# Performance work log

Measured on AMD Instinct MI355X. Metric: run time of the kernel, lower is better.

The kernel has to match this reference:

```python
import jax, jax.numpy as jnp
import numpy as np

N = 262144      # number of tokens/nodes
E = 262144      # number of dependency edges (~1 per token)
D_IN = 128
D_OUT = 128
L = 32          # number of dependency labels
R = 2 + 2 * L   # 'self', 'root', L forward labels, L reversed labels
SELF = 0        # index of 'self' weight


def setup_inputs() -> dict:
    key = jax.random.key(0)
    k1, k2, k3, k4, k5 = jax.random.split(key, 5)
    x = jax.random.normal(k1, (N, D_IN), dtype=jnp.float32)
    dep_idx = jax.random.randint(k2, (E,), 0, N)
    gov_idx = jax.random.randint(k3, (E,), 0, N)
    # edges grouped by relation label: labels occupy weight slots [2, 2+L)
    rel_idx = 2 + jnp.repeat(jnp.arange(L), E // L)
    # stacked Linear params: W[r] is [in, out] (== torch weight.T), b[r] is [out]
    W = jax.random.normal(k4, (R, D_IN, D_OUT), dtype=jnp.float32) / np.sqrt(D_IN)
    b = jax.random.normal(k5, (R, D_OUT), dtype=jnp.float32) * 0.01
    return {"x": x, "W": W, "b": b, "dep_idx": dep_idx,
            "gov_idx": gov_idx, "rel_idx": rel_idx}


def reference(x, W, b, dep_idx, gov_idx, rel_idx):
    n = x.shape[0]
    e = dep_idx.shape[0]
    eg = e // L  # edges per relation group (rel_idx is grouped/sorted)

    Wf, bf = W[2:2 + L], b[2:2 + L]           # forward-relation weights
    Wr, br = W[2 + L:2 + 2 * L], b[2 + L:]    # reversed-relation weights

    # forward messages: governor -> dependent, per-relation grouped GEMM
    xg = x[gov_idx].reshape(L, eg, D_IN)                      # [L, eg, in]
    msg_f = jnp.einsum('rei,rio->reo', xg, Wf) + bf[:, None]  # [L, eg, out]
    agg_f = jax.ops.segment_sum(msg_f.reshape(e, D_OUT), dep_idx,
                                num_segments=n)

    # reversed messages: dependent -> governor
    xd = x[dep_idx].reshape(L, eg, D_IN)
    msg_r = jnp.einsum('rei,rio->reo', xd, Wr) + br[:, None]
    agg_r = jax.ops.segment_sum(msg_r.reshape(e, D_OUT), gov_idx,
                                num_segments=n)

    # self transform for every token
    self_t = x @ W[SELF] + b[SELF]

    return jax.nn.relu(self_t + agg_f + agg_r)
```

## Files before the change

kernel.cpp:

```cpp
#include <hip/hip_runtime.h>
#include <hip/hip_bf16.h>
#include <stdint.h>

#define D_DIM 128
#define L_REL 32
#define MSG_LDW 132
#define CPB 4

typedef __attribute__((ext_vector_type(8))) short short8;
typedef __attribute__((ext_vector_type(4))) float f32x4;

__device__ __forceinline__ unsigned short f2bf(float f) {
    union { float f; unsigned u; } v; v.f = f;
    unsigned r = v.u + 0x7FFFu + ((v.u >> 16) & 1u);
    return (unsigned short)(r >> 16);
}
__device__ __forceinline__ float bf_lo(unsigned m) { return __uint_as_float(m << 16); }
__device__ __forceinline__ float bf_hi(unsigned m) { return __uint_as_float(m & 0xffff0000u); }

__device__ __forceinline__ void load_wfrag(const float* __restrict__ Wr,
                                           int w, int l15, int lq,
                                           short8 wf[2][4]) {
#pragma unroll
    for (int n = 0; n < 2; ++n) {
        int c = (w * 2 + n) * 16 + l15;
#pragma unroll
        for (int kk = 0; kk < 4; ++kk) {
            int kb = kk * 32 + lq * 8;
            short8 f;
#pragma unroll
            for (int j = 0; j < 8; ++j)
                f[j] = (short)f2bf(Wr[(size_t)(kb + j) * D_DIM + c]);
            wf[n][kk] = f;
        }
    }
}

__device__ __forceinline__ void mfma_tile(const unsigned short* xs,
                                          const short8 wf[2][4],
                                          int l15, int lq, f32x4 acc[4][2]) {
#pragma unroll
    for (int kk = 0; kk < 4; ++kk) {
        short8 a[4];
#pragma unroll
        for (int m = 0; m < 4; ++m) {
            int row = m * 16 + l15;
            unsigned byte = ((unsigned)(row * 256 + (kk * 32 + lq * 8) * 2))
                          ^ (((unsigned)(row & 7)) << 4);
            a[m] = *reinterpret_cast<const short8*>(
                       reinterpret_cast<const char*>(xs) + byte);
        }
#pragma unroll
        for (int m = 0; m < 4; ++m)
#pragma unroll
            for (int n = 0; n < 2; ++n)
                acc[m][n] = __builtin_amdgcn_mfma_f32_16x16x32_bf16(
                                a[m], wf[n][kk], acc[m][n], 0, 0, 0);
    }
}

__global__ void hist_kernel(const int* __restrict__ dep, const int* __restrict__ gov,
                            int* __restrict__ deg, int E) {
    int i = blockIdx.x * blockDim.x + threadIdx.x;
    int stride = gridDim.x * blockDim.x;
    for (; i < E; i += stride) {
        atomicAdd(&deg[dep[i]], 1);
        atomicAdd(&deg[gov[i]], 1);
    }
}

__global__ __launch_bounds__(256) void scanA_kernel(const int* __restrict__ deg,
                                                    int* __restrict__ off,
                                                    int* __restrict__ partials) {
    __shared__ int ls[256];
    const int tid = threadIdx.x;
    const int gi = blockIdx.x * 256 + tid;
    int4 v = ((const int4*)deg)[gi];
    int s = v.x + v.y + v.z + v.w;
    ls[tid] = s;
    __syncthreads();
    for (int o = 1; o < 256; o <<= 1) {
        int t = (tid >= o) ? ls[tid - o] : 0;
        __syncthreads();
        ls[tid] += t;
        __syncthreads();
    }
    int e0 = ls[tid] - s;
    int4 e; e.x = e0; e.y = e0 + v.x; e.z = e.y + v.y; e.w = e.z + v.z;
    ((int4*)off)[gi] = e;
    if (tid == 255) partials[blockIdx.x] = ls[255];
}

__global__ __launch_bounds__(256) void scanB_kernel(int* __restrict__ partials) {
    __shared__ int ls[256];
    const int tid = threadIdx.x;
    int v = partials[tid];
    ls[tid] = v;
    __syncthreads();
    for (int o = 1; o < 256; o <<= 1) {
        int t = (tid >= o) ? ls[tid - o] : 0;
        __syncthreads();
        ls[tid] += t;
        __syncthreads();
    }
    partials[tid] = ls[tid] - v;
}

__global__ __launch_bounds__(256) void scanC_kernel(int* __restrict__ off,
                                                    int* __restrict__ cur,
                                                    const int* __restrict__ partials) {
    const int p = partials[blockIdx.x];
    const int gi = blockIdx.x * 256 + threadIdx.x;
    int4 v = ((int4*)off)[gi];
    v.x += p; v.y += p; v.z += p; v.w += p;
    ((int4*)off)[gi] = v;
    ((int4*)cur)[gi] = v;
}

__global__ __launch_bounds__(256) void msg_kernel(const float* __restrict__ x,
                                                  const float* __restrict__ W,
                                                  const float* __restrict__ b,
                                                  const int* __restrict__ dep,
                                                  const int* __restrict__ gov,
                                                  int* __restrict__ cur,
                                                  unsigned* __restrict__ msg,
                                                  int eg, int blocksPerRel) {
    __shared__ __align__(16) unsigned short xs[64 * 128];
    __shared__ __align__(16) unsigned short tr[64 * MSG_LDW];
    __shared__ int sidx[CPB][64];
    __shared__ int didx[CPB][64];
    __shared__ int pos[64];

    const int tid = threadIdx.x;
    const int lane = tid & 63, w = tid >> 6;
    const int l15 = lane & 15, lq = lane >> 4;

    const int bid = blockIdx.x;
    const int vr = bid / blocksPerRel;
    const int blk = bid % blocksPerRel;
    const int r = vr & 31;
    const bool fwd = (vr < 32);
    const int* __restrict__ srcI = fwd ? gov : dep;
    const int* __restrict__ dstI = fwd ? dep : gov;

    const int ebase0 = r * eg + blk * CPB * 64;
    {
        int c = tid >> 6, t = tid & 63;
        sidx[c][t] = srcI[ebase0 + c * 64 + t];
        didx[c][t] = dstI[ebase0 + c * 64 + t];
    }

    short8 wf[2][4];
    load_wfrag(W + (size_t)(2 + vr) * D_DIM * D_DIM, w, l15, lq, wf);
    float bias[2];
#pragma unroll
    for (int n = 0; n < 2; ++n)
        bias[n] = b[(size_t)(2 + vr) * D_DIM + (w * 2 + n) * 16 + l15];

    const int srow = tid >> 5;
    const int sf4  = tid & 31;
    __syncthreads();

    float4 st[8];
#pragma unroll
    for (int it = 0; it < 8; ++it) {
        int row = it * 8 + srow;
        st[it] = *reinterpret_cast<const float4*>(
                     x + (size_t)sidx[0][row] * D_DIM + sf4 * 4);
    }
#pragma unroll
    for (int it = 0; it < 8; ++it) {
        int row = it * 8 + srow;
        unsigned lo = (unsigned)f2bf(st[it].x) | ((unsigned)f2bf(st[it].y) << 16);
        unsigned hi = (unsigned)f2bf(st[it].z) | ((unsigned)f2bf(st[it].w) << 16);
        unsigned byte = ((unsigned)(row * 256 + sf4 * 8))
                      ^ (((unsigned)(row & 7)) << 4);
        *reinterpret_cast<uint2*>(reinterpret_cast<char*>(xs) + byte) =
            make_uint2(lo, hi);
    }
    __syncthreads();

    for (int ch = 0; ch < CPB; ++ch) {
        float4 nx[8];
        if (ch + 1 < CPB) {
#pragma unroll
            for (int it = 0; it < 8; ++it) {
                int row = it * 8 + srow;
                nx[it] = *reinterpret_cast<const float4*>(
                             x + (size_t)sidx[ch + 1][row] * D_DIM + sf4 * 4);
            }
        }

        f32x4 acc[4][2];
#pragma unroll
        for (int m = 0; m < 4; ++m)
#pragma unroll
            for (int n = 0; n < 2; ++n) acc[m][n] = (f32x4){0.f, 0.f, 0.f, 0.f};
        mfma_tile(xs, wf, l15, lq, acc);

        if (tid < 64) pos[tid] = atomicAdd(&cur[didx[ch][tid]], 1);

#pragma unroll
        for (int m = 0; m < 4; ++m)
#pragma unroll
            for (int reg = 0; reg < 4; ++reg) {
                int row = m * 16 + lq * 4 + reg;
#pragma unroll
                for (int n = 0; n < 2; ++n)
                    tr[row * MSG_LDW + w * 32 + n * 16 + l15] =
                        f2bf(acc[m][n][reg] + bias[n]);
            }
        __syncthreads();

#pragma unroll
        for (int i = 0; i < 16; ++i) {
            int r0 = w * 16 + i;
            unsigned dw = *reinterpret_cast<const unsigned*>(
                              reinterpret_cast<const char*>(tr)
                              + r0 * MSG_LDW * 2 + lane * 4);
            msg[(size_t)pos[r0] * 64 + lane] = dw;
        }
        if (ch + 1 < CPB) {
#pragma unroll
            for (int it = 0; it < 8; ++it) {
                int row = it * 8 + srow;
                unsigned lo = (unsigned)f2bf(nx[it].x) | ((unsigned)f2bf(nx[it].y) << 16);
                unsigned hi = (unsigned)f2bf(nx[it].z) | ((unsigned)f2bf(nx[it].w) << 16);
                unsigned byte = ((unsigned)(row * 256 + sf4 * 8))
                              ^ (((unsigned)(row & 7)) << 4);
                *reinterpret_cast<uint2*>(reinterpret_cast<char*>(xs) + byte) =
                    make_uint2(lo, hi);
            }
            __syncthreads();
        }
    }
}

__global__ __launch_bounds__(256) void agg_kernel(const float* __restrict__ x,
                                                  const float* __restrict__ W,
                                                  const float* __restrict__ b,
                                                  const int* __restrict__ off,
                                                  const int* __restrict__ deg,
                                                  const unsigned* __restrict__ msg,
                                                  float* __restrict__ out) {
    __shared__ __align__(16) char smem[64 * MSG_LDW * 2];
    unsigned short* xs = (unsigned short*)smem;
    unsigned short* st = (unsigned short*)smem;
    __shared__ int offs[64 + 1];

    const int tid = threadIdx.x;
    const int lane = tid & 63, w = tid >> 6;
    const int l15 = lane & 15, lq = lane >> 4;
    const int base = blockIdx.x * 64;

    if (tid < 64) offs[tid] = off[base + tid];
    if (tid == 64) offs[64] = off[base + 63] + deg[base + 63];

    short8 wf[2][4];
    load_wfrag(W, w, l15, lq, wf);
    float bias[2];
#pragma unroll
    for (int n = 0; n < 2; ++n) bias[n] = b[(w * 2 + n) * 16 + l15];

#pragma unroll
    for (int it = 0; it < 8; ++it) {
        int flat = it * 256 + tid;
        int row = flat >> 5, f4 = flat & 31;
        float4 v = *reinterpret_cast<const float4*>(
                       x + (size_t)(base + row) * D_DIM + f4 * 4);
        unsigned lo = (unsigned)f2bf(v.x) | ((unsigned)f2bf(v.y) << 16);
        unsigned hi = (unsigned)f2bf(v.z) | ((unsigned)f2bf(v.w) << 16);
        unsigned byte = ((unsigned)(row * 256 + f4 * 8))
                      ^ (((unsigned)(row & 7)) << 4);
        *reinterpret_cast<uint2*>(reinterpret_cast<char*>(xs) + byte) =
            make_uint2(lo, hi);
    }
    __syncthreads();

    f32x4 acc[4][2];
#pragma unroll
    for (int m = 0; m < 4; ++m)
#pragma unroll
        for (int n = 0; n < 2; ++n) acc[m][n] = (f32x4){0.f, 0.f, 0.f, 0.f};
    mfma_tile(xs, wf, l15, lq, acc);
    __syncthreads();

#pragma unroll
    for (int m = 0; m < 4; ++m)
#pragma unroll
        for (int reg = 0; reg < 4; ++reg) {
            int row = m * 16 + lq * 4 + reg;
#pragma unroll
            for (int n = 0; n < 2; ++n)
                st[row * MSG_LDW + w * 32 + n * 16 + l15] =
                    f2bf(acc[m][n][reg] + bias[n]);
        }
    __syncthreads();

    const int nfirst = w * 16;
    int ci = 0;
    float2 accm = make_float2(0.f, 0.f);

#define FLUSH_NODE()                                                          \
    do {                                                                      \
        const unsigned sv = *reinterpret_cast<const unsigned*>(               \
            reinterpret_cast<const char*>(st)                                 \
            + (nfirst + ci) * MSG_LDW * 2 + lane * 4);                        \
        float2 so;                                                            \
        so.x = fmaxf(bf_lo(sv) + accm.x, 0.f);                                \
        so.y = fmaxf(bf_hi(sv) + accm.y, 0.f);                                \
        *reinterpret_cast<float2*>(                                           \
            out + (size_t)(base + nfirst + ci) * D_DIM + lane * 2) = so;      \
        accm.x = 0.f; accm.y = 0.f;                                           \
        ++ci;                                                                 \
    } while (0)

    const int s0 = offs[nfirst];
    const int s1 = offs[nfirst + 16];
    int nb = offs[nfirst + 1];
    int j = s0;
    const unsigned* mp = msg + (size_t)j * 64 + lane;

    for (; j + 16 <= s1; j += 16, mp += 1024) {
        unsigned v[16];
#pragma unroll
        for (int k = 0; k < 16; ++k) v[k] = mp[k * 64];
#pragma unroll
        for (int k = 0; k < 16; ++k) {
            int jj = j + k;
            while (jj >= nb) { FLUSH_NODE(); nb = offs[nfirst + ci + 1]; }
            accm.x += bf_lo(v[k]); accm.y += bf_hi(v[k]);
        }
    }
    for (; j < s1; ++j, mp += 64) {
        unsigned v = mp[0];
        while (j >= nb) { FLUSH_NODE(); nb = offs[nfirst + ci + 1]; }
        accm.x += bf_lo(v); accm.y += bf_hi(v);
    }
    while (ci < 16) FLUSH_NODE();
#undef FLUSH_NODE
}

__global__ __launch_bounds__(256) void self_kernel(const float* __restrict__ x,
                                                   const float* __restrict__ W,
                                                   const float* __restrict__ b,
                                                   float* __restrict__ out) {
    __shared__ unsigned short xs[64 * D_DIM];
    const int tid = threadIdx.x;
    const int lane = tid & 63, w = tid >> 6;
    const int l15 = lane & 15, lq = lane >> 4;
    short8 wf[2][4];
    load_wfrag(W, w, l15, lq, wf);
    float bias[2];
#pragma unroll
    for (int n = 0; n < 2; ++n) bias[n] = b[(w * 2 + n) * 16 + l15];
    const int rbase = blockIdx.x * 64;
#pragma unroll
    for (int it = 0; it < 8; ++it) {
        int flat = it * 256 + tid;
        int row = flat >> 5, f4 = flat & 31;
        float4 v = *reinterpret_cast<const float4*>(
                       x + (size_t)(rbase + row) * D_DIM + f4 * 4);
        unsigned lo = (unsigned)f2bf(v.x) | ((unsigned)f2bf(v.y) << 16);
        unsigned hi = (unsigned)f2bf(v.z) | ((unsigned)f2bf(v.w) << 16);
        unsigned byte = ((unsigned)(row * 256 + f4 * 8))
                      ^ (((unsigned)(row & 7)) << 4);
        *reinterpret_cast<uint2*>(reinterpret_cast<char*>(xs) + byte) =
            make_uint2(lo, hi);
    }
    __syncthreads();
    f32x4 acc[4][2];
#pragma unroll
    for (int m = 0; m < 4; ++m)
#pragma unroll
        for (int n = 0; n < 2; ++n) acc[m][n] = (f32x4){0.f, 0.f, 0.f, 0.f};
    mfma_tile(xs, wf, l15, lq, acc);
#pragma unroll
    for (int m = 0; m < 4; ++m)
#pragma unroll
        for (int reg = 0; reg < 4; ++reg) {
            int row = rbase + m * 16 + lq * 4 + reg;
#pragma unroll
            for (int n = 0; n < 2; ++n) {
                int c = (w * 2 + n) * 16 + l15;
                out[(size_t)row * D_DIM + c] = acc[m][n][reg] + bias[n];
            }
        }
}

__global__ __launch_bounds__(256) void edge_kernel(const float* __restrict__ x,
                                                   const float* __restrict__ W,
                                                   const float* __restrict__ b,
                                                   const int* __restrict__ dep,
                                                   const int* __restrict__ gov,
                                                   float* __restrict__ out,
                                                   int eg, int blocksPerRel) {
    __shared__ unsigned short xs[64 * D_DIM];
    __shared__ int sidx[CPB][64];
    __shared__ int didx[CPB][64];
    const int tid = threadIdx.x;
    const int lane = tid & 63, w = tid >> 6;
    const int l15 = lane & 15, lq = lane >> 4;
    const int bid = blockIdx.x;
    const int vr = bid / blocksPerRel;
    const int blk = bid % blocksPerRel;
    const int r = vr & 31;
    const bool fwd = (vr < 32);
    const int* __restrict__ srcI = fwd ? gov : dep;
    const int* __restrict__ dstI = fwd ? dep : gov;
    const int ebase0 = r * eg + blk * CPB * 64;
    {
        int c = tid >> 6, t = tid & 63;
        sidx[c][t] = srcI[ebase0 + c * 64 + t];
        didx[c][t] = dstI[ebase0 + c * 64 + t];
    }
    short8 wf[2][4];
    load_wfrag(W + (size_t)(2 + vr) * D_DIM * D_DIM, w, l15, lq, wf);
    float bias[2];
#pragma unroll
    for (int n = 0; n < 2; ++n)
        bias[n] = b[(size_t)(2 + vr) * D_DIM + (w * 2 + n) * 16 + l15];
    __syncthreads();
#pragma unroll
    for (int ch = 0; ch < CPB; ++ch) {
#pragma unroll
        for (int it = 0; it < 8; ++it) {
            int flat = it * 256 + tid;
            int row = flat >> 5, f4 = flat & 31;
            float4 v = *reinterpret_cast<const float4*>(
                           x + (size_t)sidx[ch][row] * D_DIM + f4 * 4);
            unsigned lo = (unsigned)f2bf(v.x) | ((unsigned)f2bf(v.y) << 16);
            unsigned hi = (unsigned)f2bf(v.z) | ((unsigned)f2bf(v.w) << 16);
            unsigned byte = ((unsigned)(row * 256 + f4 * 8))
                          ^ (((unsigned)(row & 7)) << 4);
            *reinterpret_cast<uint2*>(reinterpret_cast<char*>(xs) + byte) =
                make_uint2(lo, hi);
        }
        __syncthreads();
        f32x4 acc[4][2];
#pragma unroll
        for (int m = 0; m < 4; ++m)
#pragma unroll
            for (int n = 0; n < 2; ++n) acc[m][n] = (f32x4){0.f, 0.f, 0.f, 0.f};
        mfma_tile(xs, wf, l15, lq, acc);
#pragma unroll
        for (int m = 0; m < 4; ++m)
#pragma unroll
            for (int reg = 0; reg < 4; ++reg) {
                int erow = m * 16 + lq * 4 + reg;
                int dst = didx[ch][erow];
#pragma unroll
                for (int n = 0; n < 2; ++n) {
                    int c = (w * 2 + n) * 16 + l15;
                    unsafeAtomicAdd(&out[(size_t)dst * D_DIM + c],
                                    acc[m][n][reg] + bias[n]);
                }
            }
        __syncthreads();
    }
}

__global__ void relu_kernel(float* __restrict__ o, int n4) {
    int i = blockIdx.x * blockDim.x + threadIdx.x;
    int stride = gridDim.x * blockDim.x;
    float4* p = reinterpret_cast<float4*>(o);
    for (; i < n4; i += stride) {
        float4 v = p[i];
        v.x = fmaxf(v.x, 0.f); v.y = fmaxf(v.y, 0.f);
        v.z = fmaxf(v.z, 0.f); v.w = fmaxf(v.w, 0.f);
        p[i] = v;
    }
}

extern "C" void kernel_launch(void* const* d_in, const int* in_sizes, int n_in,
                              void* d_out, int out_size, void* d_ws, size_t ws_size,
                              hipStream_t stream) {
    const float* x   = (const float*)d_in[0];
    const float* W   = (const float*)d_in[1];
    const float* b   = (const float*)d_in[2];
    const int*   dep = (const int*)d_in[3];
    const int*   gov = (const int*)d_in[4];
    float* out = (float*)d_out;

    const int N  = in_sizes[0] / D_DIM;
    const int E  = in_sizes[3];
    const int eg = E / L_REL;

    const size_t msgBytes = (size_t)2 * E * 64 * sizeof(unsigned);
    const size_t need = msgBytes + (size_t)(3 * N + 256) * 4 + 4096;

    const int blocksPerRel = eg / 64 / CPB;

    if (ws_size >= need) {
        char* basep = (char*)d_ws;
        unsigned* msg = (unsigned*)basep;
        int* deg = (int*)(basep + msgBytes);
        int* off = deg + (size_t)N;
        int* cur = off + (size_t)N;
        int* partials = cur + (size_t)N;

        hipMemsetAsync(deg, 0, (size_t)N * sizeof(int), stream);
        hist_kernel<<<512, 256, 0, stream>>>(dep, gov, deg, E);
        scanA_kernel<<<N / 1024, 256, 0, stream>>>(deg, off, partials);
        scanB_kernel<<<1, 256, 0, stream>>>(partials);
        scanC_kernel<<<N / 1024, 256, 0, stream>>>(off, cur, partials);

        msg_kernel<<<64 * blocksPerRel, 256, 0, stream>>>(x, W, b, dep, gov,
                                                          cur, msg, eg,
                                                          blocksPerRel);
        agg_kernel<<<N / 64, 256, 0, stream>>>(x, W, b, off, deg, msg, out);
    } else {
        self_kernel<<<N / 64, 256, 0, stream>>>(x, W, b, out);
        edge_kernel<<<64 * blocksPerRel, 256, 0, stream>>>(x, W, b, dep, gov, out,
                                                           eg, blocksPerRel);
        relu_kernel<<<2048, 256, 0, stream>>>(out, out_size / 4);
    }
}
```

Measured before the change: 213.7 us.

## Write messages straight from MFMA registers and double-buffer staging in msg kernel

The message kernel drops the LDS transpose buffer and writes packed bf16 pairs directly from MFMA accumulators to the global message array, using a permuted column order. The x staging tile is double-buffered and the slot atomics for the next chunk are issued early, which removes one barrier per chunk. The aggregation kernel reads the same permuted layout, with its self-transform tile packed the same way and outputs written as scalar floats at permuted columns. The aim is fewer LDS round trips and syncs, at the cost of less coalesced 4-byte global stores and double the LDS for x.

```diff
diff --git a/kernel.cpp b/kernel.cpp
--- a/kernel.cpp
+++ b/kernel.cpp
@@ -4,7 +4,7 @@
 
 #define D_DIM 128
 #define L_REL 32
-#define MSG_LDW 132
+#define ST_LDW 66
 #define CPB 4
 
 typedef __attribute__((ext_vector_type(8))) short short8;
@@ -125,11 +125,10 @@
                                                   int* __restrict__ cur,
                                                   unsigned* __restrict__ msg,
                                                   int eg, int blocksPerRel) {
-    __shared__ __align__(16) unsigned short xs[64 * 128];
-    __shared__ __align__(16) unsigned short tr[64 * MSG_LDW];
+    __shared__ __align__(16) unsigned short xs[2][64 * 128];
     __shared__ int sidx[CPB][64];
     __shared__ int didx[CPB][64];
-    __shared__ int pos[64];
+    __shared__ int pos[2][64];
 
     const int tid = threadIdx.x;
     const int lane = tid & 63, w = tid >> 6;
@@ -161,26 +160,31 @@
     const int sf4  = tid & 31;
     __syncthreads();
 
-    float4 st[8];
-#pragma unroll
-    for (int it = 0; it < 8; ++it) {
-        int row = it * 8 + srow;
-        st[it] = *reinterpret_cast<const float4*>(
-                     x + (size_t)sidx[0][row] * D_DIM + sf4 * 4);
-    }
-#pragma unroll
-    for (int it = 0; it < 8; ++it) {
-        int row = it * 8 + srow;
-        unsigned lo = (unsigned)f2bf(st[it].x) | ((unsigned)f2bf(st[it].y) << 16);
-        unsigned hi = (unsigned)f2bf(st[it].z) | ((unsigned)f2bf(st[it].w) << 16);
-        unsigned byte = ((unsigned)(row * 256 + sf4 * 8))
-                      ^ (((unsigned)(row & 7)) << 4);
-        *reinterpret_cast<uint2*>(reinterpret_cast<char*>(xs) + byte) =
-            make_uint2(lo, hi);
+    {
+        float4 st0[8];
+#pragma unroll
+        for (int it = 0; it < 8; ++it) {
+            int row = it * 8 + srow;
+            st0[it] = *reinterpret_cast<const float4*>(
+                          x + (size_t)sidx[0][row] * D_DIM + sf4 * 4);
+        }
+#pragma unroll
+        for (int it = 0; it < 8; ++it) {
+            int row = it * 8 + srow;
+            unsigned lo = (unsigned)f2bf(st0[it].x) | ((unsigned)f2bf(st0[it].y) << 16);
+            unsigned hi = (unsigned)f2bf(st0[it].z) | ((unsigned)f2bf(st0[it].w) << 16);
+            unsigned byte = ((unsigned)(row * 256 + sf4 * 8))
+                          ^ (((unsigned)(row & 7)) << 4);
+            *reinterpret_cast<uint2*>(reinterpret_cast<char*>(xs[0]) + byte) =
+                make_uint2(lo, hi);
+        }
+        if (tid < 64) pos[0][tid] = atomicAdd(&cur[didx[0][tid]], 1);
     }
     __syncthreads();
 
     for (int ch = 0; ch < CPB; ++ch) {
+        const int cb = ch & 1;
+
         float4 nx[8];
         if (ch + 1 < CPB) {
 #pragma unroll
@@ -196,30 +200,18 @@
         for (int m = 0; m < 4; ++m)
 #pragma unroll
             for (int n = 0; n < 2; ++n) acc[m][n] = (f32x4){0.f, 0.f, 0.f, 0.f};
-        mfma_tile(xs, wf, l15, lq, acc);
-
-        if (tid < 64) pos[tid] = atomicAdd(&cur[didx[ch][tid]], 1);
+        mfma_tile(xs[cb], wf, l15, lq, acc);
 
 #pragma unroll
         for (int m = 0; m < 4; ++m)
 #pragma unroll
             for (int reg = 0; reg < 4; ++reg) {
                 int row = m * 16 + lq * 4 + reg;
-#pragma unroll
-                for (int n = 0; n < 2; ++n)
-                    tr[row * MSG_LDW + w * 32 + n * 16 + l15] =
-                        f2bf(acc[m][n][reg] + bias[n]);
+                unsigned dw = (unsigned)f2bf(acc[m][0][reg] + bias[0])
+                            | ((unsigned)f2bf(acc[m][1][reg] + bias[1]) << 16);
+                msg[(size_t)pos[cb][row] * 64 + w * 16 + l15] = dw;
             }
-        __syncthreads();
-
-#pragma unroll
-        for (int i = 0; i < 16; ++i) {
-            int r0 = w * 16 + i;
-            unsigned dw = *reinterpret_cast<const unsigned*>(
-                              reinterpret_cast<const char*>(tr)
-                              + r0 * MSG_LDW * 2 + lane * 4);
-            msg[(size_t)pos[r0] * 64 + lane] = dw;
-        }
+
         if (ch + 1 < CPB) {
 #pragma unroll
             for (int it = 0; it < 8; ++it) {
@@ -228,9 +220,10 @@
                 unsigned hi = (unsigned)f2bf(nx[it].z) | ((unsigned)f2bf(nx[it].w) << 16);
                 unsigned byte = ((unsigned)(row * 256 + sf4 * 8))
                               ^ (((unsigned)(row & 7)) << 4);
-                *reinterpret_cast<uint2*>(reinterpret_cast<char*>(xs) + byte) =
+                *reinterpret_cast<uint2*>(reinterpret_cast<char*>(xs[cb ^ 1]) + byte) =
                     make_uint2(lo, hi);
             }
+            if (tid < 64) pos[cb ^ 1][tid] = atomicAdd(&cur[didx[ch + 1][tid]], 1);
             __syncthreads();
         }
     }
@@ -243,9 +236,9 @@
                                                   const int* __restrict__ deg,
                                                   const unsigned* __restrict__ msg,
                                                   float* __restrict__ out) {
-    __shared__ __align__(16) char smem[64 * MSG_LDW * 2];
+    __shared__ __align__(16) char smem[64 * ST_LDW * 4];
     unsigned short* xs = (unsigned short*)smem;
-    unsigned short* st = (unsigned short*)smem;
+    unsigned* stu = (unsigned*)smem;
     __shared__ int offs[64 + 1];
 
     const int tid = threadIdx.x;
@@ -290,27 +283,23 @@
 #pragma unroll
         for (int reg = 0; reg < 4; ++reg) {
             int row = m * 16 + lq * 4 + reg;
-#pragma unroll
-            for (int n = 0; n < 2; ++n)
-                st[row * MSG_LDW + w * 32 + n * 16 + l15] =
-                    f2bf(acc[m][n][reg] + bias[n]);
+            unsigned dw = (unsigned)f2bf(acc[m][0][reg] + bias[0])
+                        | ((unsigned)f2bf(acc[m][1][reg] + bias[1]) << 16);
+            stu[row * ST_LDW + w * 16 + l15] = dw;
         }
     __syncthreads();
 
     const int nfirst = w * 16;
+    const int c0 = lq * 32 + l15;
     int ci = 0;
     float2 accm = make_float2(0.f, 0.f);
 
 #define FLUSH_NODE()                                                          \
     do {                                                                      \
-        const unsigned sv = *reinterpret_cast<const unsigned*>(               \
-            reinterpret_cast<const char*>(st)                                 \
-            + (nfirst + ci) * MSG_LDW * 2 + lane * 4);                        \
-        float2 so;                                                            \
-        so.x = fmaxf(bf_lo(sv) + accm.x, 0.f);                                \
-        so.y = fmaxf(bf_hi(sv) + accm.y, 0.f);                                \
-        *reinterpret_cast<float2*>(                                           \
-            out + (size_t)(base + nfirst + ci) * D_DIM + lane * 2) = so;      \
+        const unsigned sv = stu[(nfirst + ci) * ST_LDW + lane];               \
+        float* orow = out + (size_t)(base + nfirst + ci) * D_DIM;             \
+        orow[c0]      = fmaxf(bf_lo(sv) + accm.x, 0.f);                       \
+        orow[c0 + 16] = fmaxf(bf_hi(sv) + accm.y, 0.f);                       \
         accm.x = 0.f; accm.y = 0.f;                                           \
         ++ci;                                                                 \
     } while (0)
```

New measurement: 229.0 us. +7.2%, slower.
